# Kernel optimization log

Measured on AMD Instinct MI355X. Metric: run time of the kernel, lower is better.

Reference implementation:

```python
import jax, jax.numpy as jnp
import numpy as np

N = 50000      # nodes
E = 800000     # edges (avg degree 16)
G = 512        # graphs in batch
F_IN = 14      # raw atom features
D = 64         # hidden feats_dim after projection
M = 64         # m_dim
L = 3          # egnn layers

silu = jax.nn.silu


def setup_inputs() -> dict:
    key = jax.random.key(0)
    ks = jax.random.split(key, 32)
    s = 0.1  # weight scale
    def w(k, shape):
        return jax.random.normal(k, shape, dtype=jnp.float32) * s
    inp = {
        "x": jax.random.normal(ks[0], (N, F_IN), dtype=jnp.float32),
        "pos": jax.random.normal(ks[1], (N, 3), dtype=jnp.float32),
        "edge_index": jax.random.randint(ks[2], (2, E), 0, N, dtype=jnp.int32),
        "batch": jnp.sort(jax.random.randint(ks[3], (N,), 0, G, dtype=jnp.int32)),
        # feat projection 14 -> 64
        "proj_w": w(ks[4], (F_IN, D)), "proj_b": jnp.zeros((D,), jnp.float32),
        # per-layer EGNN params, stacked over L layers
        "edge_w1": w(ks[5], (L, 2 * D, M)), "edge_b1": jnp.zeros((L, M), jnp.float32),
        "edge_w2": w(ks[6], (L, M, M)),     "edge_b2": jnp.zeros((L, M), jnp.float32),
        "node_w1": w(ks[7], (L, D + M, M)), "node_b1": jnp.zeros((L, M), jnp.float32),
        "node_w2": w(ks[8], (L, M, D)),     "node_b2": jnp.zeros((L, D), jnp.float32),
        # readout head
        "lin1_w": w(ks[9], (D, M)),  "lin1_b": jnp.zeros((M,), jnp.float32),
        "lin2_w": w(ks[10], (M, D)), "lin2_b": jnp.zeros((D,), jnp.float32),
        "lin3_w": w(ks[11], (D, M)), "lin3_b": jnp.zeros((M,), jnp.float32),
        "lin4_w": w(ks[12], (M, 1)), "lin4_b": jnp.zeros((1,), jnp.float32),
    }
    return inp


def reference(x, pos, edge_index, batch,
              proj_w, proj_b,
              edge_w1, edge_b1, edge_w2, edge_b2,
              node_w1, node_b1, node_w2, node_b2,
              lin1_w, lin1_b, lin2_w, lin2_b, lin3_w, lin3_b, lin4_w, lin4_b):
    # feature projection (do_feat_proj since dim > num_feat)
    h = x @ proj_w + proj_b                         # [N, D]
    src, dst = edge_index[0], edge_index[1]          # x_j = source, x_i = target
    for l in range(L):
        # message: edge_mlp(concat(x_i, x_j))
        cat = jnp.concatenate([h[dst], h[src]], axis=-1)       # [E, 2D]
        m = silu(cat @ edge_w1[l] + edge_b1[l])                 # [E, M]
        m = silu(m @ edge_w2[l] + edge_b2[l])                   # [E, M]
        # aggregate: scatter-add to target nodes
        agg = jax.ops.segment_sum(m, dst, num_segments=N)       # [N, M]
        # node update: node_mlp(concat(x, m_i)) + x
        u = jnp.concatenate([h, agg], axis=-1)                  # [N, D+M]
        u = silu(u @ node_w1[l] + node_b1[l])
        h = u @ node_w2[l] + node_b2[l] + h                      # residual
    per_atom_out = h                                             # [N, D]
    o = silu(h @ lin1_w + lin1_b) @ lin2_w + lin2_b              # [N, D]
    o = jax.ops.segment_sum(o, batch, num_segments=G)            # [G, D]
    o = silu(o @ lin3_w + lin3_b) @ lin4_w + lin4_b              # [G, 1]
    return o.reshape(-1), per_atom_out
```

## Files before the change

kernel.cpp:

```cpp
#include <hip/hip_runtime.h>

#define NN 50000
#define EE 800000
#define GG 512
#define LL 3

typedef short bf16x8 __attribute__((ext_vector_type(8)));
typedef float f32x4  __attribute__((ext_vector_type(4)));

__device__ __forceinline__ float silu_f(float x) {
    return x * __builtin_amdgcn_rcpf(1.0f + __expf(-x));
}
__device__ __forceinline__ unsigned short bf16_rne(float x) {
    unsigned u = __float_as_uint(x);
    u += 0x7fffu + ((u >> 16) & 1u);
    return (unsigned short)(u >> 16);
}
__device__ __forceinline__ float bflo(unsigned u) { return __uint_as_float(u << 16); }
__device__ __forceinline__ float bfhi(unsigned u) { return __uint_as_float(u & 0xffff0000u); }
__device__ __forceinline__ f32x4 mfma16(bf16x8 a, bf16x8 b, f32x4 c) {
    return __builtin_amdgcn_mfma_f32_16x16x32_bf16(a, b, c, 0, 0, 0);
}
__device__ __forceinline__ void barrier_lgkm() {
    asm volatile("s_waitcnt lgkmcnt(0)" ::: "memory");
    __builtin_amdgcn_s_barrier();
}

__global__ __launch_bounds__(256) void hist_kernel(const int* __restrict__ ei,
                                                   int* __restrict__ deg8) {
    int e = blockIdx.x * 256 + threadIdx.x;
    if (e < EE) atomicAdd(&deg8[(e & 7) * NN + ei[EE + e]], 1);
}

__global__ __launch_bounds__(512) void scanA_kernel(const int* __restrict__ deg8,
                                                    int* __restrict__ rowptr,
                                                    int* __restrict__ bsum) {
    __shared__ int wsum[8];
    const int tid = threadIdx.x, b = blockIdx.x;
    int i = b * 512 + tid;
    int v = 0;
    if (i < NN) {
#pragma unroll
        for (int s = 0; s < 8; ++s) v += deg8[s * NN + i];
    }
    int lane = tid & 63, wid = tid >> 6;
    int x = v;
#pragma unroll
    for (int s = 1; s < 64; s <<= 1) {
        int u = __shfl_up(x, s, 64);
        if (lane >= s) x += u;
    }
    if (lane == 63) wsum[wid] = x;
    __syncthreads();
    int woff = 0;
    for (int w = 0; w < wid; ++w) woff += wsum[w];
    if (i < NN) rowptr[i] = woff + x - v;
    if (tid == 511) bsum[b] = woff + x;
}

__global__ __launch_bounds__(128) void scanB_kernel(int* __restrict__ bsum, int nb) {
    __shared__ int wsum[2];
    const int tid = threadIdx.x;
    int v = (tid < nb) ? bsum[tid] : 0;
    int lane = tid & 63, wid = tid >> 6;
    int x = v;
#pragma unroll
    for (int s = 1; s < 64; s <<= 1) {
        int u = __shfl_up(x, s, 64);
        if (lane >= s) x += u;
    }
    if (lane == 63) wsum[wid] = x;
    __syncthreads();
    int woff = (wid == 1) ? wsum[0] : 0;
    if (tid < nb) bsum[tid] = woff + x - v;
}

__global__ __launch_bounds__(512) void scanC_kernel(int* __restrict__ rowptr,
                                                    int* __restrict__ cursor8,
                                                    const int* __restrict__ deg8,
                                                    const int* __restrict__ bsum) {
    const int tid = threadIdx.x, b = blockIdx.x;
    int i = b * 512 + tid;
    if (i < NN) {
        int r = rowptr[i] + bsum[b];
        rowptr[i] = r;
        int running = r;
#pragma unroll
        for (int s = 0; s < 8; ++s) {
            cursor8[s * NN + i] = running;
            running += deg8[s * NN + i];
        }
    }
    if (i == 0) rowptr[NN] = EE;
}

__global__ __launch_bounds__(256) void scatter_kernel(const int* __restrict__ ei,
                                                      int* __restrict__ cursor8,
                                                      int2* __restrict__ epair) {
    int e = blockIdx.x * 256 + threadIdx.x;
    if (e < EE) {
        int d = ei[EE + e];
        int pos = atomicAdd(&cursor8[(e & 7) * NN + d], 1);
        epair[pos] = make_int2(ei[e], d);
    }
}

__global__ __launch_bounds__(512, 2) void pk_kernel(
    const float* __restrict__ h, const float* __restrict__ w1g,
    float* __restrict__ Pt, unsigned short* __restrict__ Pbu, int ntiles)
{
    extern __shared__ __align__(16) char smem[];
    char*  hb = smem;
    char*  wt = hb + 16384;
    float* tp = (float*)(wt + 16384);

    const int tid = threadIdx.x;
    const int l   = tid & 63;
    const int w   = tid >> 6;
    const int mi  = w >> 1;
    const int ni  = w & 1;
    const int l15 = l & 15;
    const int l4  = l >> 4;
    const int sw  = (l15 & 7) << 4;

    {
        int c = tid >> 2, kq0 = tid & 3;
#pragma unroll
        for (int hf = 0; hf < 2; ++hf) {
            int kq = kq0 + 4 * hf;
            const float* wp = w1g + (size_t)((c >> 6) * 64 + kq * 8) * 64 + (c & 63);
            bf16x8 bv;
#pragma unroll
            for (int j = 0; j < 8; ++j) bv[j] = (short)bf16_rne(wp[j * 64]);
            *(bf16x8*)(wt + c * 128 + ((kq * 16) ^ ((c & 7) << 4))) = bv;
        }
    }

    for (int tile = blockIdx.x; tile < ntiles; tile += gridDim.x) {
        const int base = tile * 128;
        __syncthreads();
        {
            int r = tid >> 2, q = tid & 3;
            int n = base + r;
            float v[16];
#pragma unroll
            for (int j = 0; j < 16; ++j) v[j] = 0.f;
            if (n < NN) {
                const float* hp = h + (size_t)64 * n + q * 16;
#pragma unroll
                for (int j = 0; j < 4; ++j) {
                    float4 t = *(const float4*)(hp + 4 * j);
                    v[4 * j] = t.x; v[4 * j + 1] = t.y;
                    v[4 * j + 2] = t.z; v[4 * j + 3] = t.w;
                }
            }
            bf16x8 b0, b1;
#pragma unroll
            for (int j = 0; j < 8; ++j) {
                b0[j] = (short)bf16_rne(v[j]);
                b1[j] = (short)bf16_rne(v[8 + j]);
            }
            int swr = (r & 7) << 4;
            *(bf16x8*)(hb + r * 128 + ((q * 32) ^ swr))      = b0;
            *(bf16x8*)(hb + r * 128 + ((q * 32 + 16) ^ swr)) = b1;
        }
        __syncthreads();
        f32x4 acc[2][4];
#pragma unroll
        for (int m = 0; m < 2; ++m)
#pragma unroll
            for (int n = 0; n < 4; ++n) acc[m][n] = (f32x4){0.f, 0.f, 0.f, 0.f};
#pragma unroll
        for (int ks = 0; ks < 2; ++ks) {
            int kb = ks * 64 + l4 * 16;
            bf16x8 af[2], bf[4];
#pragma unroll
            for (int m = 0; m < 2; ++m)
                af[m] = *(const bf16x8*)(hb + (32 * mi + 16 * m + l15) * 128 + (kb ^ sw));
#pragma unroll
            for (int n = 0; n < 4; ++n)
                bf[n] = *(const bf16x8*)(wt + (64 * ni + 16 * n + l15) * 128 + (kb ^ sw));
#pragma unroll
            for (int m = 0; m < 2; ++m)
#pragma unroll
                for (int n = 0; n < 4; ++n)
                    acc[m][n] = mfma16(af[m], bf[n], acc[m][n]);
        }
        __syncthreads();
        if (ni == 0) {
#pragma unroll
            for (int m = 0; m < 2; ++m)
#pragma unroll
                for (int n = 0; n < 4; ++n)
#pragma unroll
                    for (int r = 0; r < 4; ++r)
                        tp[(32 * mi + 16 * m + l4 * 4 + r) * 68 + 16 * n + l15] =
                            acc[m][n][r];
        }
        __syncthreads();
        {
            int r = tid >> 2, q = tid & 3;
            int n = base + r;
            if (n < NN) {
                float* op = Pt + (size_t)64 * n + q * 16;
#pragma unroll
                for (int j = 0; j < 4; ++j)
                    *(float4*)(op + 4 * j) = *(const float4*)&tp[r * 68 + q * 16 + 4 * j];
            }
        }
        __syncthreads();
        if (ni == 1) {
#pragma unroll
            for (int m = 0; m < 2; ++m)
#pragma unroll
                for (int n = 0; n < 4; ++n)
#pragma unroll
                    for (int r = 0; r < 4; ++r)
                        tp[(32 * mi + 16 * m + l4 * 4 + r) * 68 + 16 * n + l15] =
                            acc[m][n][r];
        }
        __syncthreads();
        {
            int r = tid >> 2, q = tid & 3;
            int n = base + r;
            if (n < NN) {
                unsigned uu[8];
#pragma unroll
                for (int j = 0; j < 8; ++j) {
                    float lo = tp[r * 68 + q * 16 + 2 * j];
                    float hi = tp[r * 68 + q * 16 + 2 * j + 1];
                    uu[j] = ((unsigned)bf16_rne(hi) << 16) | bf16_rne(lo);
                }
                uint4* op = (uint4*)(Pbu + (size_t)64 * n + q * 16);
                op[0] = make_uint4(uu[0], uu[1], uu[2], uu[3]);
                op[1] = make_uint4(uu[4], uu[5], uu[6], uu[7]);
            }
        }
    }
}

__global__ __launch_bounds__(512, 6) void edge_kernel(
    const float* __restrict__ Pt, const unsigned short* __restrict__ Pbu,
    const int2* __restrict__ epair,
    const float* __restrict__ b1g,
    const float* __restrict__ w2g, const float* __restrict__ b2g,
    unsigned short* __restrict__ m2g, int ntiles)
{
    extern __shared__ __align__(16) char smem[];
    char*  wt2s = smem;
    char*  m1s  = wt2s + 8192;
    float* b1s  = (float*)(m1s + 16384);
    float* b2s  = b1s + 64;

    const int tid = threadIdx.x;
    const int l   = tid & 63;
    const int w   = tid >> 6;
    const int mi  = w >> 1;
    const int ni  = w & 1;
    const int l15 = l & 15;
    const int l4  = l >> 4;
    const int g7  = tid & 7;

    {
        int c = tid >> 3, kc = tid & 7;
        const float* wp = w2g + (kc * 8) * 64 + c;
        bf16x8 bv;
#pragma unroll
        for (int j = 0; j < 8; ++j) bv[j] = (short)bf16_rne(wp[j * 64]);
        *(bf16x8*)(wt2s + c * 128 + ((kc * 16) ^ ((c & 7) << 4))) = bv;
    }
    if (tid < 64) { b1s[tid] = b1g[tid]; b2s[tid] = b2g[tid]; }

    int    ix_d[2], ix_s[2];
    float4 pf_a0[2], pf_a1[2];
    uint4  pf_pb[2];

    auto IDX = [&](int tt) {
        int eb = tt * 128;
#pragma unroll
        for (int it = 0; it < 2; ++it) {
            int e = (it * 512 + tid) >> 3;
            int2 p = epair[eb + e];
            ix_s[it] = p.x;
            ix_d[it] = p.y;
        }
    };
    auto DATA = [&]() {
#pragma unroll
        for (int it = 0; it < 2; ++it) {
            const float* pt = Pt + (size_t)64 * ix_d[it] + 8 * g7;
            pf_a0[it] = *(const float4*)pt;
            pf_a1[it] = *(const float4*)(pt + 4);
            pf_pb[it] = *(const uint4*)(Pbu + (size_t)64 * ix_s[it] + 8 * g7);
        }
    };

    int tile = blockIdx.x;
    if (tile < ntiles) { IDX(tile); DATA(); }
    if (tile + gridDim.x < ntiles) IDX(tile + gridDim.x);
    barrier_lgkm();

    for (; tile < ntiles; tile += gridDim.x) {
#pragma unroll
        for (int it = 0; it < 2; ++it) {
            int e = (it * 512 + tid) >> 3;
            float4 b0  = *(const float4*)(b1s + 8 * g7);
            float4 b1v = *(const float4*)(b1s + 8 * g7 + 4);
            float v0 = silu_f(pf_a0[it].x + bflo(pf_pb[it].x) + b0.x);
            float v1 = silu_f(pf_a0[it].y + bfhi(pf_pb[it].x) + b0.y);
            float v2 = silu_f(pf_a0[it].z + bflo(pf_pb[it].y) + b0.z);
            float v3 = silu_f(pf_a0[it].w + bfhi(pf_pb[it].y) + b0.w);
            float v4 = silu_f(pf_a1[it].x + bflo(pf_pb[it].z) + b1v.x);
            float v5 = silu_f(pf_a1[it].y + bfhi(pf_pb[it].z) + b1v.y);
            float v6 = silu_f(pf_a1[it].z + bflo(pf_pb[it].w) + b1v.z);
            float v7 = silu_f(pf_a1[it].w + bfhi(pf_pb[it].w) + b1v.w);
            uint4 o;
            o.x = ((unsigned)bf16_rne(v1) << 16) | bf16_rne(v0);
            o.y = ((unsigned)bf16_rne(v3) << 16) | bf16_rne(v2);
            o.z = ((unsigned)bf16_rne(v5) << 16) | bf16_rne(v4);
            o.w = ((unsigned)bf16_rne(v7) << 16) | bf16_rne(v6);
            *(uint4*)(m1s + e * 128 + ((g7 * 16) ^ ((e & 7) << 4))) = o;
        }
        barrier_lgkm();
        int nxt = tile + gridDim.x;
        if (nxt < ntiles) {
            DATA();
            if (nxt + gridDim.x < ntiles) IDX(nxt + gridDim.x);
        }
        f32x4 acc2[2][2];
#pragma unroll
        for (int m = 0; m < 2; ++m)
#pragma unroll
            for (int n = 0; n < 2; ++n) {
                float b = b2s[32 * ni + 16 * n + l15];
                acc2[m][n] = (f32x4){b, b, b, b};
            }
        const int sw = (l15 & 7) << 4;
#pragma unroll
        for (int ks = 0; ks < 2; ++ks) {
            int kb = ks * 64 + l4 * 16;
            bf16x8 af[2], bfr[2];
#pragma unroll
            for (int m = 0; m < 2; ++m)
                af[m] = *(const bf16x8*)(m1s + (32 * mi + 16 * m + l15) * 128 + (kb ^ sw));
#pragma unroll
            for (int n = 0; n < 2; ++n)
                bfr[n] = *(const bf16x8*)(wt2s + (32 * ni + 16 * n + l15) * 128 + (kb ^ sw));
#pragma unroll
            for (int m = 0; m < 2; ++m)
#pragma unroll
                for (int n = 0; n < 2; ++n)
                    acc2[m][n] = mfma16(af[m], bfr[n], acc2[m][n]);
        }
        unsigned short* mg = m2g + (size_t)(tile * 128) * 64;
#pragma unroll
        for (int m = 0; m < 2; ++m)
#pragma unroll
            for (int n = 0; n < 2; ++n)
#pragma unroll
                for (int r = 0; r < 4; ++r) {
                    int row = 32 * mi + 16 * m + l4 * 4 + r;
                    int col = 32 * ni + 16 * n + l15;
                    mg[row * 64 + col] = bf16_rne(silu_f(acc2[m][n][r]));
                }
        barrier_lgkm();
    }
}

__global__ __launch_bounds__(256) void agg_kernel(
    const unsigned short* __restrict__ m2g, const int* __restrict__ rowptr,
    float* __restrict__ agg)
{
    int idx = blockIdx.x * 256 + threadIdx.x;
    if (idx >= NN * 16) return;
    int n = idx >> 4, c = idx & 15;
    int e0 = rowptr[n], e1 = rowptr[n + 1];
    float a0 = 0.f, a1 = 0.f, a2 = 0.f, a3 = 0.f;
    int e = e0;
    for (; e + 4 <= e1; e += 4) {
        uint2 u0 = *(const uint2*)(m2g + (size_t)(e + 0) * 64 + 4 * c);
        uint2 u1 = *(const uint2*)(m2g + (size_t)(e + 1) * 64 + 4 * c);
        uint2 u2 = *(const uint2*)(m2g + (size_t)(e + 2) * 64 + 4 * c);
        uint2 u3 = *(const uint2*)(m2g + (size_t)(e + 3) * 64 + 4 * c);
        a0 += (bflo(u0.x) + bflo(u1.x)) + (bflo(u2.x) + bflo(u3.x));
        a1 += (bfhi(u0.x) + bfhi(u1.x)) + (bfhi(u2.x) + bfhi(u3.x));
        a2 += (bflo(u0.y) + bflo(u1.y)) + (bflo(u2.y) + bflo(u3.y));
        a3 += (bfhi(u0.y) + bfhi(u1.y)) + (bfhi(u2.y) + bfhi(u3.y));
    }
    for (; e < e1; ++e) {
        uint2 u = *(const uint2*)(m2g + (size_t)e * 64 + 4 * c);
        a0 += bflo(u.x); a1 += bfhi(u.x);
        a2 += bflo(u.y); a3 += bfhi(u.y);
    }
    *(float4*)(agg + (size_t)64 * n + 4 * c) = make_float4(a0, a1, a2, a3);
}

__global__ __launch_bounds__(512, 1) void node_mlp_kernel(
    const float* __restrict__ A, const float* __restrict__ A2,
    const float* __restrict__ w1g, const float* __restrict__ b1g,
    const float* __restrict__ w2g, const float* __restrict__ b2g,
    float* __restrict__ outp, int nrows, int ntiles)
{
    extern __shared__ float lds[];
    float* ws1  = lds;
    float* ws2  = ws1 + 8192;
    float* wb1  = ws2 + 4096;
    float* wb2  = wb1 + 64;
    float* cats = wb2 + 64;
    float* m1s  = cats + 128 * 132;

    const int tid = threadIdx.x;
    const int tr  = tid & 31;
    const int tc  = tid >> 5;

    for (int i = tid; i < 2048; i += 512)
        *(float4*)&ws1[4 * i] = *(const float4*)&w1g[4 * i];
    for (int i = tid; i < 1024; i += 512)
        *(float4*)&ws2[4 * i] = *(const float4*)&w2g[4 * i];
    if (tid < 64) { wb1[tid] = b1g[tid]; wb2[tid] = b2g[tid]; }

    for (int tile = blockIdx.x; tile < ntiles; tile += gridDim.x) {
        const int base = tile * 128;
        __syncthreads();
#pragma unroll
        for (int rep = 0; rep < 8; ++rep) {
            int idx = rep * 512 + tid;
            int r = idx >> 5, q = idx & 31;
            int n = base + r;
            float4 v = make_float4(0.f, 0.f, 0.f, 0.f);
            if (n < nrows)
                v = (q < 16) ? *(const float4*)(A + 64 * n + 4 * q)
                             : *(const float4*)(A2 + 64 * n + 4 * (q - 16));
            *(float4*)&cats[r * 132 + 4 * q] = v;
        }
        __syncthreads();
        float acc[4][4];
#pragma unroll
        for (int jj = 0; jj < 4; ++jj)
#pragma unroll
            for (int ii = 0; ii < 4; ++ii) acc[jj][ii] = wb1[4 * tc + ii];
#pragma unroll 4
        for (int k16 = 0; k16 < 32; ++k16) {
            float4 bv0 = *(const float4*)&ws1[(4 * k16 + 0) * 64 + 4 * tc];
            float4 bv1 = *(const float4*)&ws1[(4 * k16 + 1) * 64 + 4 * tc];
            float4 bv2 = *(const float4*)&ws1[(4 * k16 + 2) * 64 + 4 * tc];
            float4 bv3 = *(const float4*)&ws1[(4 * k16 + 3) * 64 + 4 * tc];
#pragma unroll
            for (int jj = 0; jj < 4; ++jj) {
                float4 av = *(const float4*)&cats[(tr + 32 * jj) * 132 + 4 * k16];
                acc[jj][0] = fmaf(av.x, bv0.x, fmaf(av.y, bv1.x, fmaf(av.z, bv2.x, fmaf(av.w, bv3.x, acc[jj][0]))));
                acc[jj][1] = fmaf(av.x, bv0.y, fmaf(av.y, bv1.y, fmaf(av.z, bv2.y, fmaf(av.w, bv3.y, acc[jj][1]))));
                acc[jj][2] = fmaf(av.x, bv0.z, fmaf(av.y, bv1.z, fmaf(av.z, bv2.z, fmaf(av.w, bv3.z, acc[jj][2]))));
                acc[jj][3] = fmaf(av.x, bv0.w, fmaf(av.y, bv1.w, fmaf(av.z, bv2.w, fmaf(av.w, bv3.w, acc[jj][3]))));
            }
        }
#pragma unroll
        for (int jj = 0; jj < 4; ++jj) {
            float4 v;
            v.x = silu_f(acc[jj][0]); v.y = silu_f(acc[jj][1]);
            v.z = silu_f(acc[jj][2]); v.w = silu_f(acc[jj][3]);
            *(float4*)&m1s[(tr + 32 * jj) * 68 + 4 * tc] = v;
        }
        __syncthreads();
        float acc2[4][4];
#pragma unroll
        for (int jj = 0; jj < 4; ++jj)
#pragma unroll
            for (int ii = 0; ii < 4; ++ii) acc2[jj][ii] = wb2[4 * tc + ii];
#pragma unroll 4
        for (int k16 = 0; k16 < 16; ++k16) {
            float4 bv0 = *(const float4*)&ws2[(4 * k16 + 0) * 64 + 4 * tc];
            float4 bv1 = *(const float4*)&ws2[(4 * k16 + 1) * 64 + 4 * tc];
            float4 bv2 = *(const float4*)&ws2[(4 * k16 + 2) * 64 + 4 * tc];
            float4 bv3 = *(const float4*)&ws2[(4 * k16 + 3) * 64 + 4 * tc];
#pragma unroll
            for (int jj = 0; jj < 4; ++jj) {
                float4 av = *(const float4*)&m1s[(tr + 32 * jj) * 68 + 4 * k16];
                acc2[jj][0] = fmaf(av.x, bv0.x, fmaf(av.y, bv1.x, fmaf(av.z, bv2.x, fmaf(av.w, bv3.x, acc2[jj][0]))));
                acc2[jj][1] = fmaf(av.x, bv0.y, fmaf(av.y, bv1.y, fmaf(av.z, bv2.y, fmaf(av.w, bv3.y, acc2[jj][1]))));
                acc2[jj][2] = fmaf(av.x, bv0.z, fmaf(av.y, bv1.z, fmaf(av.z, bv2.z, fmaf(av.w, bv3.z, acc2[jj][2]))));
                acc2[jj][3] = fmaf(av.x, bv0.w, fmaf(av.y, bv1.w, fmaf(av.z, bv2.w, fmaf(av.w, bv3.w, acc2[jj][3]))));
            }
        }
#pragma unroll
        for (int jj = 0; jj < 4; ++jj) {
            int r = tr + 32 * jj;
            int n = base + r;
            if (n < nrows) {
                float4 hold = *(const float4*)&cats[r * 132 + 4 * tc];
                *(float4*)&outp[64 * n + 4 * tc] = make_float4(
                    acc2[jj][0] + hold.x, acc2[jj][1] + hold.y,
                    acc2[jj][2] + hold.z, acc2[jj][3] + hold.w);
            }
        }
    }
}

__global__ __launch_bounds__(512, 1) void rowmlp_ro_kernel(
    const float* __restrict__ A,
    const float* __restrict__ w1g, const float* __restrict__ b1g,
    const float* __restrict__ w2g, const float* __restrict__ b2g,
    const int* __restrict__ seg, float* __restrict__ outp,
    int nrows, int ntiles)
{
    extern __shared__ float lds[];
    float* ws1  = lds;
    float* ws2  = ws1 + 4096;
    float* wb1  = ws2 + 4096;
    float* wb2  = wb1 + 64;
    float* cats = wb2 + 64;
    float* m1s  = cats + 128 * 68;
    int*   segs = (int*)(m1s + 128 * 68);

    const int tid = threadIdx.x;
    const int tr  = tid & 31;
    const int tc  = tid >> 5;

    for (int i = tid; i < 1024; i += 512) {
        *(float4*)&ws1[4 * i] = *(const float4*)&w1g[4 * i];
        *(float4*)&ws2[4 * i] = *(const float4*)&w2g[4 * i];
    }
    if (tid < 64) { wb1[tid] = b1g[tid]; wb2[tid] = b2g[tid]; }

    for (int tile = blockIdx.x; tile < ntiles; tile += gridDim.x) {
        const int base = tile * 128;
        __syncthreads();
        if (tid < 128) segs[tid] = (base + tid < nrows) ? seg[base + tid] : -1;
#pragma unroll
        for (int rep = 0; rep < 4; ++rep) {
            int idx = rep * 512 + tid;
            int r = idx >> 4, q = idx & 15;
            int n = base + r;
            float4 v = make_float4(0.f, 0.f, 0.f, 0.f);
            if (n < nrows) v = *(const float4*)(A + 64 * n + 4 * q);
            *(float4*)&cats[r * 68 + 4 * q] = v;
        }
        __syncthreads();
        float acc[4][4];
#pragma unroll
        for (int jj = 0; jj < 4; ++jj)
#pragma unroll
            for (int ii = 0; ii < 4; ++ii) acc[jj][ii] = wb1[4 * tc + ii];
#pragma unroll 4
        for (int k16 = 0; k16 < 16; ++k16) {
            float4 bv0 = *(const float4*)&ws1[(4 * k16 + 0) * 64 + 4 * tc];
            float4 bv1 = *(const float4*)&ws1[(4 * k16 + 1) * 64 + 4 * tc];
            float4 bv2 = *(const float4*)&ws1[(4 * k16 + 2) * 64 + 4 * tc];
            float4 bv3 = *(const float4*)&ws1[(4 * k16 + 3) * 64 + 4 * tc];
#pragma unroll
            for (int jj = 0; jj < 4; ++jj) {
                float4 av = *(const float4*)&cats[(tr + 32 * jj) * 68 + 4 * k16];
                acc[jj][0] = fmaf(av.x, bv0.x, fmaf(av.y, bv1.x, fmaf(av.z, bv2.x, fmaf(av.w, bv3.x, acc[jj][0]))));
                acc[jj][1] = fmaf(av.x, bv0.y, fmaf(av.y, bv1.y, fmaf(av.z, bv2.y, fmaf(av.w, bv3.y, acc[jj][1]))));
                acc[jj][2] = fmaf(av.x, bv0.z, fmaf(av.y, bv1.z, fmaf(av.z, bv2.z, fmaf(av.w, bv3.z, acc[jj][2]))));
                acc[jj][3] = fmaf(av.x, bv0.w, fmaf(av.y, bv1.w, fmaf(av.z, bv2.w, fmaf(av.w, bv3.w, acc[jj][3]))));
            }
        }
#pragma unroll
        for (int jj = 0; jj < 4; ++jj) {
            float4 v;
            v.x = silu_f(acc[jj][0]); v.y = silu_f(acc[jj][1]);
            v.z = silu_f(acc[jj][2]); v.w = silu_f(acc[jj][3]);
            *(float4*)&m1s[(tr + 32 * jj) * 68 + 4 * tc] = v;
        }
        __syncthreads();
        float acc2[4][4];
#pragma unroll
        for (int jj = 0; jj < 4; ++jj)
#pragma unroll
            for (int ii = 0; ii < 4; ++ii) acc2[jj][ii] = wb2[4 * tc + ii];
#pragma unroll 4
        for (int k16 = 0; k16 < 16; ++k16) {
            float4 bv0 = *(const float4*)&ws2[(4 * k16 + 0) * 64 + 4 * tc];
            float4 bv1 = *(const float4*)&ws2[(4 * k16 + 1) * 64 + 4 * tc];
            float4 bv2 = *(const float4*)&ws2[(4 * k16 + 2) * 64 + 4 * tc];
            float4 bv3 = *(const float4*)&ws2[(4 * k16 + 3) * 64 + 4 * tc];
#pragma unroll
            for (int jj = 0; jj < 4; ++jj) {
                float4 av = *(const float4*)&m1s[(tr + 32 * jj) * 68 + 4 * k16];
                acc2[jj][0] = fmaf(av.x, bv0.x, fmaf(av.y, bv1.x, fmaf(av.z, bv2.x, fmaf(av.w, bv3.x, acc2[jj][0]))));
                acc2[jj][1] = fmaf(av.x, bv0.y, fmaf(av.y, bv1.y, fmaf(av.z, bv2.y, fmaf(av.w, bv3.y, acc2[jj][1]))));
                acc2[jj][2] = fmaf(av.x, bv0.z, fmaf(av.y, bv1.z, fmaf(av.z, bv2.z, fmaf(av.w, bv3.z, acc2[jj][2]))));
                acc2[jj][3] = fmaf(av.x, bv0.w, fmaf(av.y, bv1.w, fmaf(av.z, bv2.w, fmaf(av.w, bv3.w, acc2[jj][3]))));
            }
        }
#pragma unroll
        for (int jj = 0; jj < 4; ++jj) {
            int r = tr + 32 * jj;
            int n = base + r;
            int gid = segs[r];
            float4 vv = (n < nrows) ? make_float4(acc2[jj][0], acc2[jj][1], acc2[jj][2], acc2[jj][3])
                                    : make_float4(0.f, 0.f, 0.f, 0.f);
            unsigned f = (tr == 0 || segs[(r > 0) ? r - 1 : 0] != gid) ? 1u : 0u;
#pragma unroll
            for (int s = 1; s < 32; s <<= 1) {
                float ux = __shfl_up(vv.x, s, 32);
                float uy = __shfl_up(vv.y, s, 32);
                float uz = __shfl_up(vv.z, s, 32);
                float uw = __shfl_up(vv.w, s, 32);
                unsigned uf = __shfl_up(f, s, 32);
                if (tr >= s) {
                    if (!f) { vv.x += ux; vv.y += uy; vv.z += uz; vv.w += uw; }
                    f |= uf;
                }
            }
            bool tail = (tr == 31) || (segs[r + 1] != gid);
            if (tail && gid >= 0) {
                float* bp = outp + 64 * gid + 4 * tc;
                atomicAdd(bp + 0, vv.x); atomicAdd(bp + 1, vv.y);
                atomicAdd(bp + 2, vv.z); atomicAdd(bp + 3, vv.w);
            }
        }
    }
}

__global__ __launch_bounds__(256) void proj_kernel(
    const float* __restrict__ x, const float* __restrict__ w,
    const float* __restrict__ b, float* __restrict__ h, int n)
{
    int i = blockIdx.x * 256 + threadIdx.x;
    if (i >= n * 64) return;
    int node = i >> 6, j = i & 63;
    const float* xr = x + node * 14;
    float acc = b[j];
#pragma unroll
    for (int k = 0; k < 14; ++k) acc = fmaf(xr[k], w[k * 64 + j], acc);
    h[i] = acc;
}

__global__ __launch_bounds__(256) void head_kernel(
    const float* __restrict__ gsum,
    const float* __restrict__ w3, const float* __restrict__ b3,
    const float* __restrict__ w4, const float* __restrict__ b4,
    float* __restrict__ out, int g_count)
{
    int wid  = (blockIdx.x * 256 + threadIdx.x) >> 6;
    int lane = threadIdx.x & 63;
    if (wid >= g_count) return;
    float v = gsum[wid * 64 + lane];
    float t = b3[lane];
#pragma unroll
    for (int k = 0; k < 64; ++k) {
        float a = __shfl(v, k, 64);
        t = fmaf(a, w3[k * 64 + lane], t);
    }
    t = silu_f(t);
    float r = t * w4[lane];
#pragma unroll
    for (int off = 32; off; off >>= 1) r += __shfl_down(r, off, 64);
    if (lane == 0) out[wid] = r + b4[0];
}

extern "C" void kernel_launch(void* const* d_in, const int* in_sizes, int n_in,
                              void* d_out, int out_size, void* d_ws, size_t ws_size,
                              hipStream_t stream)
{
    const float* x      = (const float*)d_in[0];
    const int*   ei     = (const int*)d_in[2];
    const int*   batch  = (const int*)d_in[3];
    const float* proj_w = (const float*)d_in[4];
    const float* proj_b = (const float*)d_in[5];
    const float* ew1 = (const float*)d_in[6];
    const float* eb1 = (const float*)d_in[7];
    const float* ew2 = (const float*)d_in[8];
    const float* eb2 = (const float*)d_in[9];
    const float* nw1 = (const float*)d_in[10];
    const float* nb1 = (const float*)d_in[11];
    const float* nw2 = (const float*)d_in[12];
    const float* nb2 = (const float*)d_in[13];
    const float* l1w = (const float*)d_in[14]; const float* l1b = (const float*)d_in[15];
    const float* l2w = (const float*)d_in[16]; const float* l2b = (const float*)d_in[17];
    const float* l3w = (const float*)d_in[18]; const float* l3b = (const float*)d_in[19];
    const float* l4w = (const float*)d_in[20]; const float* l4b = (const float*)d_in[21];

    float* out  = (float*)d_out;
    float* h    = out + GG;

    unsigned short* m2g = (unsigned short*)d_ws;
    float* gsum = (float*)(m2g + (size_t)EE * 64);
    float* Pt   = gsum + (size_t)GG * 64;
    unsigned short* Pbu = (unsigned short*)(Pt + (size_t)NN * 64);
    int* deg8    = (int*)(Pbu + (size_t)NN * 64);
    int* rowptr  = deg8 + 8 * NN;
    int* cursor8 = rowptr + NN + 1;
    int2* epair  = (int2*)(((uintptr_t)(cursor8 + 8 * NN) + 15) & ~(uintptr_t)15);
    int* bsum    = (int*)(epair + EE);
    float* agg   = Pt;

    const size_t edge_lds = 8192 + 16384 + 256 + 256;
    const size_t pk_lds   = 16384 + 16384 + 34816;
    const size_t node_lds = (size_t)(8192 + 4096 + 128 + 128 * 132 + 128 * 68) * 4;
    const size_t ro_lds   = (size_t)(4096 + 4096 + 128 + 128 * 68 + 128 * 68) * 4 + 128 * 4;

    (void)hipFuncSetAttribute((const void*)edge_kernel,
                              hipFuncAttributeMaxDynamicSharedMemorySize, (int)edge_lds);
    (void)hipFuncSetAttribute((const void*)pk_kernel,
                              hipFuncAttributeMaxDynamicSharedMemorySize, (int)pk_lds);
    (void)hipFuncSetAttribute((const void*)node_mlp_kernel,
                              hipFuncAttributeMaxDynamicSharedMemorySize, (int)node_lds);
    (void)hipFuncSetAttribute((const void*)rowmlp_ro_kernel,
                              hipFuncAttributeMaxDynamicSharedMemorySize, (int)ro_lds);

    const int nb = (NN + 511) / 512;
    hipMemsetAsync(deg8, 0, (size_t)8 * NN * sizeof(int), stream);
    hipMemsetAsync(gsum, 0, (size_t)GG * 64 * sizeof(float), stream);
    hist_kernel<<<(EE + 255) / 256, 256, 0, stream>>>(ei, deg8);
    scanA_kernel<<<nb, 512, 0, stream>>>(deg8, rowptr, bsum);
    scanB_kernel<<<1, 128, 0, stream>>>(bsum, nb);
    scanC_kernel<<<nb, 512, 0, stream>>>(rowptr, cursor8, deg8, bsum);
    scatter_kernel<<<(EE + 255) / 256, 256, 0, stream>>>(ei, cursor8, epair);

    proj_kernel<<<(NN * 64 + 255) / 256, 256, 0, stream>>>(x, proj_w, proj_b, h, NN);

    const int etiles = EE / 128;
    const int ntiles = (NN + 127) / 128;
    for (int l = 0; l < LL; ++l) {
        pk_kernel<<<ntiles, 512, pk_lds, stream>>>(h, ew1 + l * 8192, Pt, Pbu, ntiles);
        edge_kernel<<<1024, 512, edge_lds, stream>>>(
            Pt, Pbu, epair, eb1 + l * 64, ew2 + l * 4096, eb2 + l * 64,
            m2g, etiles);
        agg_kernel<<<(NN * 16 + 255) / 256, 256, 0, stream>>>(m2g, rowptr, agg);
        node_mlp_kernel<<<196, 512, node_lds, stream>>>(
            h, agg, nw1 + l * 8192, nb1 + l * 64, nw2 + l * 4096, nb2 + l * 64,
            h, NN, ntiles);
    }
    rowmlp_ro_kernel<<<196, 512, ro_lds, stream>>>(
        h, l1w, l1b, l2w, l2b, batch, gsum, NN, ntiles);
    head_kernel<<<GG / 4, 256, 0, stream>>>(gsum, l3w, l3b, l4w, l4b, out, GG);
}
```

Measured before the change: 464.6 us.

## Rewrite node MLP kernel with bf16 MFMA and swizzled LDS tiles

Replaces the fp32 FMA-based node update MLP with a bf16 MFMA 16x16x32 implementation. Weights are converted to bf16 and stored transposed in XOR-swizzled shared memory, and h/agg tiles are converted to bf16 on load. The fp32 second-layer output is staged through shared memory so the residual add and store are coalesced. This cuts ALU time in the node MLP at the cost of bf16 rounding of h, agg and the hidden activations, plus an extra reload of h from global for the residual.

```diff
diff --git a/kernel.cpp b/kernel.cpp
--- a/kernel.cpp
+++ b/kernel.cpp
@@ -395,102 +395,172 @@
     *(float4*)(agg + (size_t)64 * n + 4 * c) = make_float4(a0, a1, a2, a3);
 }
 
-__global__ __launch_bounds__(512, 1) void node_mlp_kernel(
-    const float* __restrict__ A, const float* __restrict__ A2,
+__global__ __launch_bounds__(512, 1) void node_mfma_kernel(
+    const float* __restrict__ h, const float* __restrict__ agg,
     const float* __restrict__ w1g, const float* __restrict__ b1g,
     const float* __restrict__ w2g, const float* __restrict__ b2g,
-    float* __restrict__ outp, int nrows, int ntiles)
+    float* __restrict__ outp, int ntiles)
 {
-    extern __shared__ float lds[];
-    float* ws1  = lds;
-    float* ws2  = ws1 + 8192;
-    float* wb1  = ws2 + 4096;
-    float* wb2  = wb1 + 64;
-    float* cats = wb2 + 64;
-    float* m1s  = cats + 128 * 132;
+    extern __shared__ __align__(16) char smem[];
+    char*  hbA = smem;
+    char*  hbB = hbA + 16384;
+    char*  wtA = hbB + 16384;
+    char*  wtB = wtA + 8192;
+    char*  wt2 = wtB + 8192;
+    char*  m1s = wt2 + 8192;
+    float* tp  = (float*)(m1s + 16384);
+    float* b1s = (float*)((char*)tp + 34816);
+    float* b2s = b1s + 64;
 
     const int tid = threadIdx.x;
-    const int tr  = tid & 31;
-    const int tc  = tid >> 5;
-
-    for (int i = tid; i < 2048; i += 512)
-        *(float4*)&ws1[4 * i] = *(const float4*)&w1g[4 * i];
-    for (int i = tid; i < 1024; i += 512)
-        *(float4*)&ws2[4 * i] = *(const float4*)&w2g[4 * i];
-    if (tid < 64) { wb1[tid] = b1g[tid]; wb2[tid] = b2g[tid]; }
+    const int l   = tid & 63;
+    const int w   = tid >> 6;
+    const int mi  = w >> 1;
+    const int ni  = w & 1;
+    const int l15 = l & 15;
+    const int l4  = l >> 4;
+    const int sw  = (l15 & 7) << 4;
+
+    {
+        int c = tid >> 3, kc = tid & 7;
+        const float* wpA = w1g + (kc * 8) * 64 + c;
+        const float* wpB = w1g + (64 + kc * 8) * 64 + c;
+        const float* wp2 = w2g + (kc * 8) * 64 + c;
+        bf16x8 bA, bB, b2v;
+#pragma unroll
+        for (int j = 0; j < 8; ++j) {
+            bA[j]  = (short)bf16_rne(wpA[j * 64]);
+            bB[j]  = (short)bf16_rne(wpB[j * 64]);
+            b2v[j] = (short)bf16_rne(wp2[j * 64]);
+        }
+        int off = c * 128 + ((kc * 16) ^ ((c & 7) << 4));
+        *(bf16x8*)(wtA + off) = bA;
+        *(bf16x8*)(wtB + off) = bB;
+        *(bf16x8*)(wt2 + off) = b2v;
+    }
+    if (tid < 64) { b1s[tid] = b1g[tid]; b2s[tid] = b2g[tid]; }
 
     for (int tile = blockIdx.x; tile < ntiles; tile += gridDim.x) {
         const int base = tile * 128;
         __syncthreads();
-#pragma unroll
-        for (int rep = 0; rep < 8; ++rep) {
-            int idx = rep * 512 + tid;
-            int r = idx >> 5, q = idx & 31;
+        {
+            int r = tid >> 2, q = tid & 3;
             int n = base + r;
-            float4 v = make_float4(0.f, 0.f, 0.f, 0.f);
-            if (n < nrows)
-                v = (q < 16) ? *(const float4*)(A + 64 * n + 4 * q)
-                             : *(const float4*)(A2 + 64 * n + 4 * (q - 16));
-            *(float4*)&cats[r * 132 + 4 * q] = v;
-        }
-        __syncthreads();
-        float acc[4][4];
-#pragma unroll
-        for (int jj = 0; jj < 4; ++jj)
-#pragma unroll
-            for (int ii = 0; ii < 4; ++ii) acc[jj][ii] = wb1[4 * tc + ii];
-#pragma unroll 4
-        for (int k16 = 0; k16 < 32; ++k16) {
-            float4 bv0 = *(const float4*)&ws1[(4 * k16 + 0) * 64 + 4 * tc];
-            float4 bv1 = *(const float4*)&ws1[(4 * k16 + 1) * 64 + 4 * tc];
-            float4 bv2 = *(const float4*)&ws1[(4 * k16 + 2) * 64 + 4 * tc];
-            float4 bv3 = *(const float4*)&ws1[(4 * k16 + 3) * 64 + 4 * tc];
-#pragma unroll
-            for (int jj = 0; jj < 4; ++jj) {
-                float4 av = *(const float4*)&cats[(tr + 32 * jj) * 132 + 4 * k16];
-                acc[jj][0] = fmaf(av.x, bv0.x, fmaf(av.y, bv1.x, fmaf(av.z, bv2.x, fmaf(av.w, bv3.x, acc[jj][0]))));
-                acc[jj][1] = fmaf(av.x, bv0.y, fmaf(av.y, bv1.y, fmaf(av.z, bv2.y, fmaf(av.w, bv3.y, acc[jj][1]))));
-                acc[jj][2] = fmaf(av.x, bv0.z, fmaf(av.y, bv1.z, fmaf(av.z, bv2.z, fmaf(av.w, bv3.z, acc[jj][2]))));
-                acc[jj][3] = fmaf(av.x, bv0.w, fmaf(av.y, bv1.w, fmaf(av.z, bv2.w, fmaf(av.w, bv3.w, acc[jj][3]))));
-            }
-        }
-#pragma unroll
-        for (int jj = 0; jj < 4; ++jj) {
-            float4 v;
-            v.x = silu_f(acc[jj][0]); v.y = silu_f(acc[jj][1]);
-            v.z = silu_f(acc[jj][2]); v.w = silu_f(acc[jj][3]);
-            *(float4*)&m1s[(tr + 32 * jj) * 68 + 4 * tc] = v;
-        }
-        __syncthreads();
-        float acc2[4][4];
-#pragma unroll
-        for (int jj = 0; jj < 4; ++jj)
-#pragma unroll
-            for (int ii = 0; ii < 4; ++ii) acc2[jj][ii] = wb2[4 * tc + ii];
-#pragma unroll 4
-        for (int k16 = 0; k16 < 16; ++k16) {
-            float4 bv0 = *(const float4*)&ws2[(4 * k16 + 0) * 64 + 4 * tc];
-            float4 bv1 = *(const float4*)&ws2[(4 * k16 + 1) * 64 + 4 * tc];
-            float4 bv2 = *(const float4*)&ws2[(4 * k16 + 2) * 64 + 4 * tc];
-            float4 bv3 = *(const float4*)&ws2[(4 * k16 + 3) * 64 + 4 * tc];
-#pragma unroll
-            for (int jj = 0; jj < 4; ++jj) {
-                float4 av = *(const float4*)&m1s[(tr + 32 * jj) * 68 + 4 * k16];
-                acc2[jj][0] = fmaf(av.x, bv0.x, fmaf(av.y, bv1.x, fmaf(av.z, bv2.x, fmaf(av.w, bv3.x, acc2[jj][0]))));
-                acc2[jj][1] = fmaf(av.x, bv0.y, fmaf(av.y, bv1.y, fmaf(av.z, bv2.y, fmaf(av.w, bv3.y, acc2[jj][1]))));
-                acc2[jj][2] = fmaf(av.x, bv0.z, fmaf(av.y, bv1.z, fmaf(av.z, bv2.z, fmaf(av.w, bv3.z, acc2[jj][2]))));
-                acc2[jj][3] = fmaf(av.x, bv0.w, fmaf(av.y, bv1.w, fmaf(av.z, bv2.w, fmaf(av.w, bv3.w, acc2[jj][3]))));
-            }
-        }
-#pragma unroll
-        for (int jj = 0; jj < 4; ++jj) {
-            int r = tr + 32 * jj;
+            int swr = (r & 7) << 4;
+#pragma unroll
+            for (int srcsel = 0; srcsel < 2; ++srcsel) {
+                const float* src = srcsel ? agg : h;
+                char* dst = srcsel ? hbB : hbA;
+                float v[16];
+#pragma unroll
+                for (int j = 0; j < 16; ++j) v[j] = 0.f;
+                if (n < NN) {
+                    const float* hp = src + (size_t)64 * n + q * 16;
+#pragma unroll
+                    for (int j = 0; j < 4; ++j) {
+                        float4 t = *(const float4*)(hp + 4 * j);
+                        v[4 * j] = t.x; v[4 * j + 1] = t.y;
+                        v[4 * j + 2] = t.z; v[4 * j + 3] = t.w;
+                    }
+                }
+                bf16x8 c0, c1;
+#pragma unroll
+                for (int j = 0; j < 8; ++j) {
+                    c0[j] = (short)bf16_rne(v[j]);
+                    c1[j] = (short)bf16_rne(v[8 + j]);
+                }
+                *(bf16x8*)(dst + r * 128 + ((q * 32) ^ swr))      = c0;
+                *(bf16x8*)(dst + r * 128 + ((q * 32 + 16) ^ swr)) = c1;
+            }
+        }
+        __syncthreads();
+        f32x4 acc[2][2];
+#pragma unroll
+        for (int m = 0; m < 2; ++m)
+#pragma unroll
+            for (int n = 0; n < 2; ++n) {
+                float b = b1s[32 * ni + 16 * n + l15];
+                acc[m][n] = (f32x4){b, b, b, b};
+            }
+#pragma unroll
+        for (int half = 0; half < 2; ++half) {
+            const char* hb = half ? hbB : hbA;
+            const char* wt = half ? wtB : wtA;
+#pragma unroll
+            for (int ks = 0; ks < 2; ++ks) {
+                int kb = ks * 64 + l4 * 16;
+                bf16x8 af[2], bf[2];
+#pragma unroll
+                for (int m = 0; m < 2; ++m)
+                    af[m] = *(const bf16x8*)(hb + (32 * mi + 16 * m + l15) * 128 + (kb ^ sw));
+#pragma unroll
+                for (int n = 0; n < 2; ++n)
+                    bf[n] = *(const bf16x8*)(wt + (32 * ni + 16 * n + l15) * 128 + (kb ^ sw));
+#pragma unroll
+                for (int m = 0; m < 2; ++m)
+#pragma unroll
+                    for (int n = 0; n < 2; ++n)
+                        acc[m][n] = mfma16(af[m], bf[n], acc[m][n]);
+            }
+        }
+#pragma unroll
+        for (int m = 0; m < 2; ++m)
+#pragma unroll
+            for (int n = 0; n < 2; ++n)
+#pragma unroll
+                for (int r = 0; r < 4; ++r) {
+                    int row = 32 * mi + 16 * m + l4 * 4 + r;
+                    int col = 32 * ni + 16 * n + l15;
+                    *(unsigned short*)(m1s + row * 128 + ((col * 2) ^ ((row & 7) << 4))) =
+                        bf16_rne(silu_f(acc[m][n][r]));
+                }
+        __syncthreads();
+        f32x4 acc2[2][2];
+#pragma unroll
+        for (int m = 0; m < 2; ++m)
+#pragma unroll
+            for (int n = 0; n < 2; ++n) {
+                float b = b2s[32 * ni + 16 * n + l15];
+                acc2[m][n] = (f32x4){b, b, b, b};
+            }
+#pragma unroll
+        for (int ks = 0; ks < 2; ++ks) {
+            int kb = ks * 64 + l4 * 16;
+            bf16x8 af[2], bfr[2];
+#pragma unroll
+            for (int m = 0; m < 2; ++m)
+                af[m] = *(const bf16x8*)(m1s + (32 * mi + 16 * m + l15) * 128 + (kb ^ sw));
+#pragma unroll
+            for (int n = 0; n < 2; ++n)
+                bfr[n] = *(const bf16x8*)(wt2 + (32 * ni + 16 * n + l15) * 128 + (kb ^ sw));
+#pragma unroll
+            for (int m = 0; m < 2; ++m)
+#pragma unroll
+                for (int n = 0; n < 2; ++n)
+                    acc2[m][n] = mfma16(af[m], bfr[n], acc2[m][n]);
+        }
+#pragma unroll
+        for (int m = 0; m < 2; ++m)
+#pragma unroll
+            for (int n = 0; n < 2; ++n)
+#pragma unroll
+                for (int r = 0; r < 4; ++r)
+                    tp[(32 * mi + 16 * m + l4 * 4 + r) * 68 + 32 * ni + 16 * n + l15] =
+                        acc2[m][n][r];
+        __syncthreads();
+        {
+            int r = tid >> 2, q = tid & 3;
             int n = base + r;
-            if (n < nrows) {
-                float4 hold = *(const float4*)&cats[r * 132 + 4 * tc];
-                *(float4*)&outp[64 * n + 4 * tc] = make_float4(
-                    acc2[jj][0] + hold.x, acc2[jj][1] + hold.y,
-                    acc2[jj][2] + hold.z, acc2[jj][3] + hold.w);
+            if (n < NN) {
+                const float* hp = h + (size_t)64 * n + q * 16;
+                float* op = outp + (size_t)64 * n + q * 16;
+#pragma unroll
+                for (int j = 0; j < 4; ++j) {
+                    float4 hv = *(const float4*)(hp + 4 * j);
+                    const float* tv = &tp[r * 68 + q * 16 + 4 * j];
+                    *(float4*)(op + 4 * j) = make_float4(
+                        tv[0] + hv.x, tv[1] + hv.y, tv[2] + hv.z, tv[3] + hv.w);
+                }
             }
         }
     }
@@ -689,14 +759,14 @@
 
     const size_t edge_lds = 8192 + 16384 + 256 + 256;
     const size_t pk_lds   = 16384 + 16384 + 34816;
-    const size_t node_lds = (size_t)(8192 + 4096 + 128 + 128 * 132 + 128 * 68) * 4;
+    const size_t node_lds = 16384 * 3 + 8192 * 3 + 34816 + 512;
     const size_t ro_lds   = (size_t)(4096 + 4096 + 128 + 128 * 68 + 128 * 68) * 4 + 128 * 4;
 
     (void)hipFuncSetAttribute((const void*)edge_kernel,
                               hipFuncAttributeMaxDynamicSharedMemorySize, (int)edge_lds);
     (void)hipFuncSetAttribute((const void*)pk_kernel,
                               hipFuncAttributeMaxDynamicSharedMemorySize, (int)pk_lds);
-    (void)hipFuncSetAttribute((const void*)node_mlp_kernel,
+    (void)hipFuncSetAttribute((const void*)node_mfma_kernel,
                               hipFuncAttributeMaxDynamicSharedMemorySize, (int)node_lds);
     (void)hipFuncSetAttribute((const void*)rowmlp_ro_kernel,
                               hipFuncAttributeMaxDynamicSharedMemorySize, (int)ro_lds);
@@ -720,9 +790,9 @@
             Pt, Pbu, epair, eb1 + l * 64, ew2 + l * 4096, eb2 + l * 64,
             m2g, etiles);
         agg_kernel<<<(NN * 16 + 255) / 256, 256, 0, stream>>>(m2g, rowptr, agg);
-        node_mlp_kernel<<<196, 512, node_lds, stream>>>(
+        node_mfma_kernel<<<196, 512, node_lds, stream>>>(
             h, agg, nw1 + l * 8192, nb1 + l * 64, nw2 + l * 4096, nb2 + l * 64,
-            h, NN, ntiles);
+            h, ntiles);
     }
     rowmlp_ro_kernel<<<196, 512, ro_lds, stream>>>(
         h, l1w, l1b, l2w, l2b, batch, gsum, NN, ntiles);
```

Measured after the change: 424.9 us, median of 2. 8.6% less time.
